# Kernel tuning notes

Measured on AMD Instinct MI355X. Metric: run time of the kernel, lower is better.

## Reference

```python
import jax, jax.numpy as jnp
import numpy as np

B, S, D, H, W = 2, 2048, 1024, 16, 128
HD = D // H
EPS = 1e-5
NEG = -1e9


def setup_inputs() -> dict:
    key = jax.random.key(0)
    ks = jax.random.split(key, 6)
    sd = 1.0 / np.sqrt(D)
    return {
        "x": jax.random.normal(ks[0], (B, S, D), jnp.float32),
        "Wq": jax.random.normal(ks[1], (D, D), jnp.float32) * sd,
        "bq": jnp.zeros((D,), jnp.float32),
        "Wk": jax.random.normal(ks[2], (D, D), jnp.float32) * sd,
        "bk": jnp.zeros((D,), jnp.float32),
        "Wv": jax.random.normal(ks[3], (D, D), jnp.float32) * sd,
        "bv": jnp.zeros((D,), jnp.float32),
        "Wo": jax.random.normal(ks[4], (D, D), jnp.float32) * sd,
        "bo": jnp.zeros((D,), jnp.float32),
        "gamma": jnp.ones((D,), jnp.float32),
        "beta": jnp.zeros((D,), jnp.float32),
    }


def _local_causal_mask(seq_len, window):
    pos = jnp.arange(seq_len)
    qp = pos[:, None]
    kp = pos[None, :]
    return (jnp.abs(qp - kp) < window) & (qp >= kp)  # [S, S] bool


def reference(x, Wq, bq, Wk, bk, Wv, bv, Wo, bo, gamma, beta):
    scale = 1.0 / np.sqrt(HD)
    # projections -> [B, H, S, HD]
    def split_heads(t):
        return t.reshape(B, S, H, HD).transpose(0, 2, 1, 3)

    q = split_heads(x @ Wq + bq)
    k = split_heads(x @ Wk + bk)
    v = split_heads(x @ Wv + bv)

    scores = jnp.einsum("bhqd,bhkd->bhqk", q, k) * scale  # [B,H,S,S]
    mask = _local_causal_mask(S, W)
    scores = jnp.where(mask[None, None, :, :], scores, NEG)
    attn = jax.nn.softmax(scores, axis=-1)
    out = jnp.einsum("bhqk,bhkd->bhqd", attn, v)  # [B,H,S,HD]
    out = out.transpose(0, 2, 1, 3).reshape(B, S, D)
    out = out @ Wo + bo

    # residual + LayerNorm(eps=1e-5)
    y = x + out
    mu = jnp.mean(y, axis=-1, keepdims=True)
    var = jnp.mean(jnp.square(y - mu), axis=-1, keepdims=True)
    y = (y - mu) * jax.lax.rsqrt(var + EPS) * gamma + beta
    return y
```

## Files before the change

kernel.cpp:

```cpp
#include <hip/hip_runtime.h>
#include <hip/hip_bf16.h>

typedef __hip_bfloat16 bf16;
typedef float f32x4 __attribute__((ext_vector_type(4)));
typedef short bf16x8 __attribute__((ext_vector_type(8)));
typedef int   int4v  __attribute__((ext_vector_type(4)));

constexpr int Bb = 2, Ss = 2048, Dd = 1024, Hh = 16, Ww = 128, HDd = 64;
constexpr int Mrows = Bb * Ss;
constexpr int NTk = Dd / 64;

__device__ __forceinline__ void gload16(const void* g, void* l) {
  __builtin_amdgcn_global_load_lds(
      (const __attribute__((address_space(1))) void*)g,
      (__attribute__((address_space(3))) void*)l, 16, 0, 0);
}

__device__ __forceinline__ f32x4 mfma16(bf16x8 a, bf16x8 b, f32x4 c) {
  return __builtin_amdgcn_mfma_f32_16x16x32_bf16(a, b, c, 0, 0, 0);
}

__global__ __launch_bounds__(256) void convert_bf16_k(const float* __restrict__ in,
                                                      bf16* __restrict__ out) {
  size_t i = (size_t)blockIdx.x * 256 + threadIdx.x;
  float4 v = reinterpret_cast<const float4*>(in)[i];
  union { bf16 b[4]; ushort4 u; } cv;
  cv.b[0] = __float2bfloat16(v.x);
  cv.b[1] = __float2bfloat16(v.y);
  cv.b[2] = __float2bfloat16(v.z);
  cv.b[3] = __float2bfloat16(v.w);
  reinterpret_cast<ushort4*>(out)[i] = cv.u;
}

__global__ __launch_bounds__(256) void transpose_w4_k(const float* __restrict__ W0,
                                                      const float* __restrict__ W1,
                                                      const float* __restrict__ W2,
                                                      const float* __restrict__ W3,
                                                      bf16* __restrict__ out) {
  const float* Win = (blockIdx.z == 0) ? W0 : (blockIdx.z == 1) ? W1
                     : (blockIdx.z == 2) ? W2 : W3;
  bf16* o = out + (size_t)blockIdx.z * Dd * Dd;
  __shared__ float tile[32][33];
  int bx = blockIdx.x, by = blockIdx.y;
  int tx = threadIdx.x & 31, ty = threadIdx.x >> 5;
#pragma unroll
  for (int i = 0; i < 4; ++i)
    tile[ty + i * 8][tx] = Win[(size_t)(by * 32 + ty + i * 8) * Dd + bx * 32 + tx];
  __syncthreads();
#pragma unroll
  for (int i = 0; i < 4; ++i)
    o[(size_t)(bx * 32 + ty + i * 8) * Dd + by * 32 + tx] =
        __float2bfloat16(tile[tx][ty + i * 8]);
}

__device__ __forceinline__ void gemm_core8(const bf16* __restrict__ A,
                                           const bf16* __restrict__ Bt,
                                           int bm, int bn,
                                           bf16* lds, f32x4 acc[2][4]) {
  const int t = threadIdx.x;
  const int lane = t & 63, w = t >> 6;
  const int wr = w >> 1, wc = w & 1;
  const int l15 = lane & 15, l16 = lane >> 4;
  const bf16* Arow0 = A + (size_t)bm * 128 * Dd;
  const bf16* Brow0 = Bt + (size_t)bn * 128 * Dd;

  auto stage = [&](int buf, int kt) {
#pragma unroll
    for (int i = 0; i < 2; ++i) {
      int ci = i * 512 + t;
      int row = ci >> 3, pc = ci & 7;
      int sc = pc ^ (row & 7);
      gload16(Arow0 + (size_t)row * Dd + kt * 64 + sc * 8, lds + buf * 16384 + ci * 8);
      gload16(Brow0 + (size_t)row * Dd + kt * 64 + sc * 8, lds + buf * 16384 + 8192 + ci * 8);
    }
  };

  stage(0, 0);
  __syncthreads();
  int buf = 0;
  for (int kt = 0; kt < NTk; ++kt) {
    if (kt + 1 < NTk) stage(buf ^ 1, kt + 1);
    bf16x8 af[2][2], bfr[4][2];
    const bf16* Ab = lds + buf * 16384;
    const bf16* Bb = Ab + 8192;
#pragma unroll
    for (int m = 0; m < 2; ++m) {
      int row = wr * 32 + m * 16 + l15;
#pragma unroll
      for (int kk = 0; kk < 2; ++kk)
        af[m][kk] = *reinterpret_cast<const bf16x8*>(
            Ab + row * 64 + (((kk * 4 + l16) ^ (row & 7)) * 8));
    }
#pragma unroll
    for (int n = 0; n < 4; ++n) {
      int row = wc * 64 + n * 16 + l15;
#pragma unroll
      for (int kk = 0; kk < 2; ++kk)
        bfr[n][kk] = *reinterpret_cast<const bf16x8*>(
            Bb + row * 64 + (((kk * 4 + l16) ^ (row & 7)) * 8));
    }
    __builtin_amdgcn_s_setprio(1);
#pragma unroll
    for (int m = 0; m < 2; ++m)
#pragma unroll
      for (int n = 0; n < 4; ++n) {
        acc[m][n] = mfma16(af[m][0], bfr[n][0], acc[m][n]);
        acc[m][n] = mfma16(af[m][1], bfr[n][1], acc[m][n]);
      }
    __builtin_amdgcn_s_setprio(0);
    __syncthreads();
    buf ^= 1;
  }
}

__global__ __launch_bounds__(512) void gemm_qkv8w(const bf16* __restrict__ A,
                                                  const bf16* __restrict__ Wt3,
                                                  const float* __restrict__ bq,
                                                  const float* __restrict__ bk,
                                                  const float* __restrict__ bv,
                                                  bf16* __restrict__ Qh,
                                                  bf16* __restrict__ Kh,
                                                  bf16* __restrict__ Vt) {
  __shared__ __align__(16) bf16 lds[32768];
  f32x4 acc[2][4] = {};
  int id = blockIdx.x;
  int wg = (id & 7) * 96 + (id >> 3);
  int bm = wg / 24, bn = wg % 24;
  gemm_core8(A, Wt3, bm, bn, lds, acc);

  const int lane = threadIdx.x & 63, w = threadIdx.x >> 6;
  const int wr = w >> 1, wc = w & 1, l15 = lane & 15, l16 = lane >> 4;
  const int p = bn >> 3;
  const int c0w = (bn & 7) * 128 + wc * 64;
  const int h = c0w >> 6;

  if (p < 2) {
    bf16 (*rep)[72] = reinterpret_cast<bf16(*)[72]>(lds + w * (16 * 72));
    bf16* dst = p ? Kh : Qh;
    const float* bp = p ? bk : bq;
    float bi[4];
#pragma unroll
    for (int n = 0; n < 4; ++n) bi[n] = bp[c0w + n * 16 + l15];
#pragma unroll
    for (int m = 0; m < 2; ++m) {
#pragma unroll
      for (int n = 0; n < 4; ++n)
#pragma unroll
        for (int r = 0; r < 4; ++r)
          rep[l16 * 4 + r][n * 16 + l15] = __float2bfloat16(acc[m][n][r] + bi[n]);
      int rrow = lane >> 2, rch = lane & 3;
      int sg = bm * 128 + wr * 32 + m * 16 + rrow;
      int b = sg >> 11, sl = sg & (Ss - 1);
      bf16* base = dst + (((size_t)(b * Hh + h)) * Ss + sl) * HDd;
      bf16x8 v0 = *reinterpret_cast<const bf16x8*>(&rep[rrow][rch * 8]);
      bf16x8 v1 = *reinterpret_cast<const bf16x8*>(&rep[rrow][(rch + 4) * 8]);
      *reinterpret_cast<bf16x8*>(base + rch * 8) = v0;
      *reinterpret_cast<bf16x8*>(base + (rch + 4) * 8) = v1;
    }
  } else {
#pragma unroll
    for (int n = 0; n < 4; ++n) {
      int col = c0w + n * 16 + l15;
      int hh = col >> 6, hd = col & (HDd - 1);
      float bi = bv[col];
#pragma unroll
      for (int m = 0; m < 2; ++m) {
        int s0 = bm * 128 + wr * 32 + m * 16 + l16 * 4;
        int b = s0 >> 11, sl = s0 & (Ss - 1);
        union { ushort4 u; ushort e[4]; } pk;
#pragma unroll
        for (int r = 0; r < 4; ++r) {
          bf16 tb = __float2bfloat16(acc[m][n][r] + bi);
          pk.e[r] = *reinterpret_cast<ushort*>(&tb);
        }
        *reinterpret_cast<ushort4*>(&Vt[(((size_t)(b * Hh + hh)) * HDd + hd) * Ss + sl]) = pk.u;
      }
    }
  }
}

__global__ __launch_bounds__(512) void gemm_o8w(const bf16* __restrict__ AO,
                                                const bf16* __restrict__ WtO,
                                                const float* __restrict__ bo,
                                                const float* __restrict__ resid,
                                                float* __restrict__ out) {
  __shared__ __align__(16) bf16 lds[32768];
  f32x4 acc[2][4] = {};
  int id = blockIdx.x;
  int wg = (id & 7) * 32 + (id >> 3);
  int bm = wg >> 3, bn = wg & 7;
  gemm_core8(AO, WtO, bm, bn, lds, acc);

  const int lane = threadIdx.x & 63, w = threadIdx.x >> 6;
  const int wr = w >> 1, wc = w & 1, l15 = lane & 15, l16 = lane >> 4;
#pragma unroll
  for (int m = 0; m < 2; ++m)
#pragma unroll
    for (int n = 0; n < 4; ++n) {
      int col = bn * 128 + wc * 64 + n * 16 + l15;
      float bi = bo[col];
#pragma unroll
      for (int r = 0; r < 4; ++r) {
        int row = bm * 128 + wr * 32 + m * 16 + l16 * 4 + r;
        size_t idx = (size_t)row * Dd + col;
        out[idx] = acc[m][n][r] + bi + resid[idx];
      }
    }
}

__global__ __launch_bounds__(256) void attn_local(const bf16* __restrict__ Q,
                                                  const bf16* __restrict__ K,
                                                  const bf16* __restrict__ Vt,
                                                  bf16* __restrict__ AO) {
  __shared__ bf16 Ps[4][16][200];
  const int t = threadIdx.x, lane = t & 63, w = t >> 6;
  const int l15 = lane & 15, l16 = lane >> 4;
  const int qb = blockIdx.x, h = blockIdx.y, b = blockIdx.z;
  const int q0 = qb * 64, kstart = q0 - 128;
  const bf16* Qp = Q + ((size_t)(b * Hh + h)) * Ss * HDd;
  const bf16* Kp = K + ((size_t)(b * Hh + h)) * Ss * HDd;
  const bf16* Vp = Vt + ((size_t)(b * Hh + h)) * HDd * Ss;

  const int qrow = q0 + w * 16 + l15;
  bf16x8 aq0 = *reinterpret_cast<const bf16x8*>(Qp + (size_t)qrow * HDd + l16 * 8);
  bf16x8 aq1 = *reinterpret_cast<const bf16x8*>(Qp + (size_t)qrow * HDd + 32 + l16 * 8);

  f32x4 sc[9];
  __builtin_amdgcn_s_setprio(1);
#pragma unroll
  for (int j = 0; j < 9; ++j) {
    int key = kstart + (w + j) * 16 + l15;
    int kc = key < 0 ? 0 : key;
    bf16x8 bk0 = *reinterpret_cast<const bf16x8*>(Kp + (size_t)kc * HDd + l16 * 8);
    bf16x8 bk1 = *reinterpret_cast<const bf16x8*>(Kp + (size_t)kc * HDd + 32 + l16 * 8);
    f32x4 s = {};
    s = mfma16(aq0, bk0, s);
    s = mfma16(aq1, bk1, s);
    sc[j] = s;
  }
  __builtin_amdgcn_s_setprio(0);

  const int c0 = w >> 1;
  bf16x8 vpre[3][4];
#pragma unroll
  for (int cc = 0; cc < 3; ++cc) {
    int kk = kstart + (c0 + cc) * 32 + l16 * 8;
    int kc = kk < 0 ? 0 : kk;
#pragma unroll
    for (int ht = 0; ht < 4; ++ht)
      vpre[cc][ht] = *reinterpret_cast<const bf16x8*>(Vp + (size_t)(ht * 16 + l15) * Ss + kc);
  }

  const float scale = 0.125f;
  float mrow[4], ssum[4], inv[4];
  int qg[4];
#pragma unroll
  for (int r = 0; r < 4; ++r) { mrow[r] = -1e30f; qg[r] = q0 + w * 16 + l16 * 4 + r; }
#pragma unroll
  for (int j = 0; j < 9; ++j) {
    int kg = kstart + (w + j) * 16 + l15;
#pragma unroll
    for (int r = 0; r < 4; ++r) {
      bool valid = (kg >= 0) && (kg <= qg[r]) && (qg[r] - kg < Ww);
      float v = valid ? sc[j][r] * scale : -1e9f;
      sc[j][r] = v;
      mrow[r] = fmaxf(mrow[r], v);
    }
  }
#pragma unroll
  for (int r = 0; r < 4; ++r)
#pragma unroll
    for (int off = 1; off < 16; off <<= 1)
      mrow[r] = fmaxf(mrow[r], __shfl_xor(mrow[r], off));
#pragma unroll
  for (int r = 0; r < 4; ++r) ssum[r] = 0.f;
#pragma unroll
  for (int j = 0; j < 9; ++j)
#pragma unroll
    for (int r = 0; r < 4; ++r) {
      float p = __expf(sc[j][r] - mrow[r]);
      sc[j][r] = p;
      ssum[r] += p;
    }
#pragma unroll
  for (int r = 0; r < 4; ++r)
#pragma unroll
    for (int off = 1; off < 16; off <<= 1)
      ssum[r] += __shfl_xor(ssum[r], off);
#pragma unroll
  for (int r = 0; r < 4; ++r) inv[r] = 1.f / ssum[r];

#pragma unroll
  for (int j = 0; j < 9; ++j)
#pragma unroll
    for (int r = 0; r < 4; ++r)
      Ps[w][l16 * 4 + r][(w + j) * 16 + l15] = __float2bfloat16(sc[j][r]);
  {
    int ktz = (w & 1) ? (w - 1) : (w + 9);
    bf16 z16 = __float2bfloat16(0.f);
#pragma unroll
    for (int r = 0; r < 4; ++r)
      Ps[w][l16 * 4 + r][ktz * 16 + l15] = z16;
  }

  f32x4 o[4] = {};
  __builtin_amdgcn_s_setprio(1);
#pragma unroll
  for (int cc = 0; cc < 5; ++cc) {
    int c = c0 + cc;
    bf16x8 pf = *reinterpret_cast<const bf16x8*>(&Ps[w][l15][c * 32 + l16 * 8]);
    if (cc < 3) {
#pragma unroll
      for (int ht = 0; ht < 4; ++ht)
        o[ht] = mfma16(pf, vpre[cc][ht], o[ht]);
    } else {
      int kk = kstart + c * 32 + l16 * 8;
      int kc = kk < 0 ? 0 : kk;
#pragma unroll
      for (int ht = 0; ht < 4; ++ht) {
        bf16x8 vf = *reinterpret_cast<const bf16x8*>(Vp + (size_t)(ht * 16 + l15) * Ss + kc);
        o[ht] = mfma16(pf, vf, o[ht]);
      }
    }
  }
  __builtin_amdgcn_s_setprio(0);

#pragma unroll
  for (int ht = 0; ht < 4; ++ht)
#pragma unroll
    for (int r = 0; r < 4; ++r) {
      int qw = q0 + w * 16 + l16 * 4 + r;
      int col = h * HDd + ht * 16 + l15;
      AO[(size_t)(b * Ss + qw) * Dd + col] = __float2bfloat16(o[ht][r] * inv[r]);
    }
}

__global__ __launch_bounds__(256) void ln_inplace(float* __restrict__ y,
                                                  const float* __restrict__ gamma,
                                                  const float* __restrict__ beta) {
  int row = blockIdx.x;
  float* yr = y + (size_t)row * Dd;
  float4 v = reinterpret_cast<const float4*>(yr)[threadIdx.x];
  float s = v.x + v.y + v.z + v.w;
  float s2 = v.x * v.x + v.y * v.y + v.z * v.z + v.w * v.w;
#pragma unroll
  for (int off = 1; off < 64; off <<= 1) {
    s += __shfl_xor(s, off);
    s2 += __shfl_xor(s2, off);
  }
  __shared__ float r1[4], r2[4];
  int w = threadIdx.x >> 6;
  if ((threadIdx.x & 63) == 0) { r1[w] = s; r2[w] = s2; }
  __syncthreads();
  s = r1[0] + r1[1] + r1[2] + r1[3];
  s2 = r2[0] + r2[1] + r2[2] + r2[3];
  float mu = s * (1.f / Dd);
  float var = s2 * (1.f / Dd) - mu * mu;
  float rs = rsqrtf(var + 1e-5f);
  float4 g = reinterpret_cast<const float4*>(gamma)[threadIdx.x];
  float4 be = reinterpret_cast<const float4*>(beta)[threadIdx.x];
  float4 o;
  o.x = (v.x - mu) * rs * g.x + be.x;
  o.y = (v.y - mu) * rs * g.y + be.y;
  o.z = (v.z - mu) * rs * g.z + be.z;
  o.w = (v.w - mu) * rs * g.w + be.w;
  reinterpret_cast<float4*>(yr)[threadIdx.x] = o;
}

extern "C" void kernel_launch(void* const* d_in, const int* in_sizes, int n_in,
                              void* d_out, int out_size, void* d_ws, size_t ws_size,
                              hipStream_t stream) {
  const float* x     = (const float*)d_in[0];
  const float* Wq    = (const float*)d_in[1];
  const float* bq    = (const float*)d_in[2];
  const float* Wk    = (const float*)d_in[3];
  const float* bk    = (const float*)d_in[4];
  const float* Wv    = (const float*)d_in[5];
  const float* bv    = (const float*)d_in[6];
  const float* Wo    = (const float*)d_in[7];
  const float* bo    = (const float*)d_in[8];
  const float* gamma = (const float*)d_in[9];
  const float* beta  = (const float*)d_in[10];
  float* out = (float*)d_out;

  char* ws = (char*)d_ws;
  bf16* xb  = (bf16*)(ws + (size_t)0);
  bf16* Wt3 = (bf16*)(ws + ((size_t)8  << 20));
  bf16* WtO = (bf16*)(ws + ((size_t)14 << 20));
  bf16* Qh  = (bf16*)(ws + ((size_t)16 << 20));
  bf16* Kh  = (bf16*)(ws + ((size_t)24 << 20));
  bf16* Vt  = (bf16*)(ws + ((size_t)32 << 20));
  bf16* AO  = (bf16*)(ws + ((size_t)40 << 20));

  convert_bf16_k<<<Mrows * Dd / (256 * 4), 256, 0, stream>>>(x, xb);
  transpose_w4_k<<<dim3(32, 32, 4), 256, 0, stream>>>(Wq, Wk, Wv, Wo, Wt3);

  gemm_qkv8w<<<768, 512, 0, stream>>>(xb, Wt3, bq, bk, bv, Qh, Kh, Vt);

  attn_local<<<dim3(Ss / 64, Hh, Bb), 256, 0, stream>>>(Qh, Kh, Vt, AO);

  gemm_o8w<<<256, 512, 0, stream>>>(AO, WtO, bo, x, out);
  ln_inplace<<<Mrows, 256, 0, stream>>>(out, gamma, beta);
}
```

Measured before the change: 98.83 us.

## Stage K and V tiles in swizzled LDS with 128-query attention blocks

The local attention kernel now processes 128 queries per block with 8 waves. It stages the 256-key K window and the transposed V window into LDS through async global-to-LDS loads, using an XOR swizzle to avoid bank conflicts. Waves then read K and V fragments from LDS instead of each wave issuing redundant global loads, and the halo overhead per query is lower than with 64-query blocks. The cost is more LDS per block (about 64KB plus P scratch), which limits occupancy, plus a block-wide barrier before compute.

```diff
diff --git a/kernel.cpp b/kernel.cpp
--- a/kernel.cpp
+++ b/kernel.cpp
@@ -208,48 +208,61 @@
     }
 }
 
-__global__ __launch_bounds__(256) void attn_local(const bf16* __restrict__ Q,
-                                                  const bf16* __restrict__ K,
-                                                  const bf16* __restrict__ Vt,
-                                                  bf16* __restrict__ AO) {
-  __shared__ bf16 Ps[4][16][200];
+__global__ __launch_bounds__(512) void attn_local2(const bf16* __restrict__ Q,
+                                                   const bf16* __restrict__ K,
+                                                   const bf16* __restrict__ Vt,
+                                                   bf16* __restrict__ AO) {
+  __shared__ __align__(16) bf16 Kl[256 * 64];
+  __shared__ __align__(16) bf16 Vl[64 * 256];
+  __shared__ bf16 Ps[8][16][168];
   const int t = threadIdx.x, lane = t & 63, w = t >> 6;
   const int l15 = lane & 15, l16 = lane >> 4;
   const int qb = blockIdx.x, h = blockIdx.y, b = blockIdx.z;
-  const int q0 = qb * 64, kstart = q0 - 128;
+  const int q0 = qb * 128, kstart = q0 - 128;
   const bf16* Qp = Q + ((size_t)(b * Hh + h)) * Ss * HDd;
   const bf16* Kp = K + ((size_t)(b * Hh + h)) * Ss * HDd;
   const bf16* Vp = Vt + ((size_t)(b * Hh + h)) * HDd * Ss;
 
+#pragma unroll
+  for (int i = 0; i < 4; ++i) {
+    int ci = i * 512 + t;
+    int row = ci >> 3, pc = ci & 7;
+    int sc = pc ^ (row & 7);
+    int key = kstart + row;
+    if (key < 0) key = 0;
+    gload16(Kp + (size_t)key * HDd + sc * 8, (bf16*)Kl + ci * 8);
+  }
+#pragma unroll
+  for (int i = 0; i < 4; ++i) {
+    int ci = i * 512 + t;
+    int row = ci >> 5, pc = ci & 31;
+    int sc = pc ^ (row & 7);
+    int k8 = kstart + sc * 8;
+    if (k8 < 0) k8 = 0;
+    gload16(Vp + (size_t)row * Ss + k8, (bf16*)Vl + ci * 8);
+  }
+
   const int qrow = q0 + w * 16 + l15;
   bf16x8 aq0 = *reinterpret_cast<const bf16x8*>(Qp + (size_t)qrow * HDd + l16 * 8);
   bf16x8 aq1 = *reinterpret_cast<const bf16x8*>(Qp + (size_t)qrow * HDd + 32 + l16 * 8);
 
-  f32x4 sc[9];
+  __syncthreads();
+
+  f32x4 sc9[9];
   __builtin_amdgcn_s_setprio(1);
 #pragma unroll
   for (int j = 0; j < 9; ++j) {
-    int key = kstart + (w + j) * 16 + l15;
-    int kc = key < 0 ? 0 : key;
-    bf16x8 bk0 = *reinterpret_cast<const bf16x8*>(Kp + (size_t)kc * HDd + l16 * 8);
-    bf16x8 bk1 = *reinterpret_cast<const bf16x8*>(Kp + (size_t)kc * HDd + 32 + l16 * 8);
+    int krow = (w + j) * 16 + l15;
+    bf16x8 bk0 = *reinterpret_cast<const bf16x8*>(
+        Kl + krow * 64 + (((0 + l16) ^ (krow & 7)) * 8));
+    bf16x8 bk1 = *reinterpret_cast<const bf16x8*>(
+        Kl + krow * 64 + (((4 + l16) ^ (krow & 7)) * 8));
     f32x4 s = {};
     s = mfma16(aq0, bk0, s);
     s = mfma16(aq1, bk1, s);
-    sc[j] = s;
+    sc9[j] = s;
   }
   __builtin_amdgcn_s_setprio(0);
-
-  const int c0 = w >> 1;
-  bf16x8 vpre[3][4];
-#pragma unroll
-  for (int cc = 0; cc < 3; ++cc) {
-    int kk = kstart + (c0 + cc) * 32 + l16 * 8;
-    int kc = kk < 0 ? 0 : kk;
-#pragma unroll
-    for (int ht = 0; ht < 4; ++ht)
-      vpre[cc][ht] = *reinterpret_cast<const bf16x8*>(Vp + (size_t)(ht * 16 + l15) * Ss + kc);
-  }
 
   const float scale = 0.125f;
   float mrow[4], ssum[4], inv[4];
@@ -262,8 +275,8 @@
 #pragma unroll
     for (int r = 0; r < 4; ++r) {
       bool valid = (kg >= 0) && (kg <= qg[r]) && (qg[r] - kg < Ww);
-      float v = valid ? sc[j][r] * scale : -1e9f;
-      sc[j][r] = v;
+      float v = valid ? sc9[j][r] * scale : -1e9f;
+      sc9[j][r] = v;
       mrow[r] = fmaxf(mrow[r], v);
     }
   }
@@ -278,8 +291,8 @@
   for (int j = 0; j < 9; ++j)
 #pragma unroll
     for (int r = 0; r < 4; ++r) {
-      float p = __expf(sc[j][r] - mrow[r]);
-      sc[j][r] = p;
+      float p = __expf(sc9[j][r] - mrow[r]);
+      sc9[j][r] = p;
       ssum[r] += p;
     }
 #pragma unroll
@@ -291,36 +304,32 @@
   for (int r = 0; r < 4; ++r) inv[r] = 1.f / ssum[r];
 
 #pragma unroll
-  for (int j = 0; j < 9; ++j)
+  for (int j = 0; j < 9; ++j) {
+    int lt = j + (w & 1);
 #pragma unroll
     for (int r = 0; r < 4; ++r)
-      Ps[w][l16 * 4 + r][(w + j) * 16 + l15] = __float2bfloat16(sc[j][r]);
+      Ps[w][l16 * 4 + r][lt * 16 + l15] = __float2bfloat16(sc9[j][r]);
+  }
   {
-    int ktz = (w & 1) ? (w - 1) : (w + 9);
+    int ltz = (w & 1) ? 0 : 9;
     bf16 z16 = __float2bfloat16(0.f);
 #pragma unroll
     for (int r = 0; r < 4; ++r)
-      Ps[w][l16 * 4 + r][ktz * 16 + l15] = z16;
+      Ps[w][l16 * 4 + r][ltz * 16 + l15] = z16;
   }
 
   f32x4 o[4] = {};
   __builtin_amdgcn_s_setprio(1);
 #pragma unroll
   for (int cc = 0; cc < 5; ++cc) {
-    int c = c0 + cc;
-    bf16x8 pf = *reinterpret_cast<const bf16x8*>(&Ps[w][l15][c * 32 + l16 * 8]);
-    if (cc < 3) {
-#pragma unroll
-      for (int ht = 0; ht < 4; ++ht)
-        o[ht] = mfma16(pf, vpre[cc][ht], o[ht]);
-    } else {
-      int kk = kstart + c * 32 + l16 * 8;
-      int kc = kk < 0 ? 0 : kk;
-#pragma unroll
-      for (int ht = 0; ht < 4; ++ht) {
-        bf16x8 vf = *reinterpret_cast<const bf16x8*>(Vp + (size_t)(ht * 16 + l15) * Ss + kc);
-        o[ht] = mfma16(pf, vf, o[ht]);
-      }
+    bf16x8 pf = *reinterpret_cast<const bf16x8*>(&Ps[w][l15][cc * 32 + l16 * 8]);
+    int gch = ((w >> 1) + cc) * 4 + l16;
+#pragma unroll
+    for (int ht = 0; ht < 4; ++ht) {
+      int vrow = ht * 16 + l15;
+      bf16x8 vf = *reinterpret_cast<const bf16x8*>(
+          Vl + vrow * 256 + ((gch ^ (vrow & 7)) * 8));
+      o[ht] = mfma16(pf, vf, o[ht]);
     }
   }
   __builtin_amdgcn_s_setprio(0);
@@ -397,7 +406,7 @@
 
   gemm_qkv8w<<<768, 512, 0, stream>>>(xb, Wt3, bq, bk, bv, Qh, Kh, Vt);
 
-  attn_local<<<dim3(Ss / 64, Hh, Bb), 256, 0, stream>>>(Qh, Kh, Vt, AO);
+  attn_local2<<<dim3(Ss / 128, Hh, Bb), 512, 0, stream>>>(Qh, Kh, Vt, AO);
 
   gemm_o8w<<<256, 512, 0, stream>>>(AO, WtO, bo, x, out);
   ln_inplace<<<Mrows, 256, 0, stream>>>(out, gamma, beta);
```

Result: faster. 90.92 us (-8.0%).
